# Kernel optimization log

Measured on AMD Instinct MI355X. Metric: run time of the kernel, lower is better.

The kernel has to match this reference:

```python
import jax, jax.numpy as jnp
import numpy as np

N = 50000
E = 800000
D = 128


def setup_inputs() -> dict:
    key = jax.random.key(0)
    ks = jax.random.split(key, 8)
    X = jax.random.normal(ks[0], (N, D), dtype=jnp.float32)
    edge_index = jax.random.randint(ks[1], (2, E), 0, N, dtype=jnp.int64)
    edge_weight = jax.random.uniform(ks[2], (E,), dtype=jnp.float32)
    # GCN weight (glorot-ish) and single-layer LSTM params (PyTorch layout).
    gcn_weight = jax.random.normal(ks[3], (D, D), dtype=jnp.float32) / np.sqrt(D)
    w_ih = jax.random.normal(ks[4], (4 * D, D), dtype=jnp.float32) / np.sqrt(D)
    w_hh = jax.random.normal(ks[5], (4 * D, D), dtype=jnp.float32) / np.sqrt(D)
    b_ih = jax.random.normal(ks[6], (4 * D,), dtype=jnp.float32) / np.sqrt(D)
    b_hh = jax.random.normal(ks[7], (4 * D,), dtype=jnp.float32) / np.sqrt(D)
    return {"X": X, "edge_index": edge_index, "edge_weight": edge_weight,
            "gcn_weight": gcn_weight, "w_ih": w_ih, "w_hh": w_hh,
            "b_ih": b_ih, "b_hh": b_hh}


def _lstm_evolve_weight(W, w_ih, w_hh, b_ih, b_hh):
    # One LSTM step on the weight matrix: seq_len=1, batch=D, input=D, h0=c0=0.
    # h0 contribution is zero but kept so w_hh participates in the graph.
    gates = W @ w_ih.T + jnp.zeros_like(W) @ w_hh.T + b_ih + b_hh  # [D, 4D]
    i, f, g, o = jnp.split(gates, 4, axis=-1)  # PyTorch gate order i,f,g,o
    c = jax.nn.sigmoid(i) * jnp.tanh(g)        # f * c0 = 0
    h = jax.nn.sigmoid(o) * jnp.tanh(c)
    return h  # new [D, D] weight


def reference(X, edge_index, edge_weight, gcn_weight, w_ih, w_hh, b_ih, b_hh):
    W = _lstm_evolve_weight(gcn_weight, w_ih, w_hh, b_ih, b_hh)
    n = X.shape[0]
    # GCNConv: add self-loops (weight 1), symmetric normalization.
    loop = jnp.arange(n, dtype=edge_index.dtype)
    row = jnp.concatenate([edge_index[0], loop])   # sources
    col = jnp.concatenate([edge_index[1], loop])   # targets (aggregation)
    ew = jnp.concatenate([edge_weight, jnp.ones((n,), dtype=edge_weight.dtype)])
    deg = jax.ops.segment_sum(ew, col, num_segments=n)
    dinv = jnp.where(deg > 0, jax.lax.rsqrt(jnp.maximum(deg, 1e-30)), 0.0)
    norm = dinv[row] * ew * dinv[col]              # [E+N]
    xw = X @ W                                     # [N, D] dense transform first
    out = jax.ops.segment_sum(norm[:, None] * xw[row], col, num_segments=n)
    return out
```

## Files before the change

kernel.cpp:

```cpp
#include <hip/hip_runtime.h>
#include <math.h>

#define N_NODES 50000
#define N_EDGES 800000
#define DIM 128
#define PART_SZ 6250
#define SUBCAP 32

typedef __attribute__((ext_vector_type(8))) short bf16x8;
typedef __attribute__((ext_vector_type(4))) float f32x4;
typedef __attribute__((ext_vector_type(4))) int i32x4;

__device__ inline unsigned short f2bf(float f) {
  unsigned int u = __builtin_bit_cast(unsigned int, f);
  u = (u + 0x7FFFu + ((u >> 16) & 1u)) >> 16;
  return (unsigned short)u;
}
__device__ inline float bflo(unsigned int v) {
  return __builtin_bit_cast(float, v << 16);
}
__device__ inline float bfhi(unsigned int v) {
  return __builtin_bit_cast(float, v & 0xffff0000u);
}

__global__ __launch_bounds__(256) void lstm_evolve(
    const float* __restrict__ gcn, const float* __restrict__ w_ih,
    const float* __restrict__ b_ih, const float* __restrict__ b_hh,
    unsigned short* __restrict__ Wt) {
  int idx = blockIdx.x * 256 + threadIdx.x;
  int r = idx >> 7;
  int c = idx & 127;
  const float4* g_row = (const float4*)(gcn + r * DIM);
  const float4* wi = (const float4*)(w_ih + (long)c * DIM);
  const float4* wg = (const float4*)(w_ih + (long)(c + 256) * DIM);
  const float4* wo = (const float4*)(w_ih + (long)(c + 384) * DIM);
  float ai = 0.f, ag = 0.f, ao = 0.f;
#pragma unroll 8
  for (int k = 0; k < DIM / 4; ++k) {
    float4 gv = g_row[k];
    float4 iv = wi[k], gg = wg[k], ov = wo[k];
    ai += gv.x * iv.x + gv.y * iv.y + gv.z * iv.z + gv.w * iv.w;
    ag += gv.x * gg.x + gv.y * gg.y + gv.z * gg.z + gv.w * gg.w;
    ao += gv.x * ov.x + gv.y * ov.y + gv.z * ov.z + gv.w * ov.w;
  }
  ai += b_ih[c] + b_hh[c];
  ag += b_ih[c + 256] + b_hh[c + 256];
  ao += b_ih[c + 384] + b_hh[c + 384];
  float si = 1.f / (1.f + expf(-ai));
  float so = 1.f / (1.f + expf(-ao));
  float cc = si * tanhf(ag);
  float h = so * tanhf(cc);
  Wt[c * DIM + r] = f2bf(h);
}

__global__ __launch_bounds__(256) void init_cursor(int* __restrict__ cursor) {
  int i = blockIdx.x * 256 + threadIdx.x;
  if (i < N_NODES * 2) cursor[i] = 0;
}

__device__ inline void put_edge(int c, long e, int src, float w,
                                int* __restrict__ cursor,
                                unsigned int* __restrict__ bkt) {
  int sub = (int)e & 1;
  int pos = atomicAdd(&cursor[c * 2 + sub], 1);
  if (pos < SUBCAP) {
    unsigned int pk = ((unsigned int)src << 16) | (unsigned int)f2bf(w);
    bkt[(long)c * 64 + sub * SUBCAP + pos] = pk;
  }
}

__global__ __launch_bounds__(256) void fill_buckets(
    const int* __restrict__ rows, const int* __restrict__ cols,
    const float* __restrict__ ew, int* __restrict__ cursor,
    unsigned int* __restrict__ bkt) {
  int part = blockIdx.x & 7;
  int lo = part * PART_SZ;
  int hi = lo + PART_SZ;
  long e0 = ((long)(blockIdx.x >> 3)) * 1024 + threadIdx.x * 4;
  if (e0 >= N_EDGES) return;
  i32x4 c = __builtin_nontemporal_load((const i32x4*)(cols + e0));
  if (c.x >= lo && c.x < hi) {
    int s = __builtin_nontemporal_load(rows + e0 + 0);
    float w = __builtin_nontemporal_load(ew + e0 + 0);
    put_edge(c.x, e0 + 0, s, w, cursor, bkt);
  }
  if (c.y >= lo && c.y < hi) {
    int s = __builtin_nontemporal_load(rows + e0 + 1);
    float w = __builtin_nontemporal_load(ew + e0 + 1);
    put_edge(c.y, e0 + 1, s, w, cursor, bkt);
  }
  if (c.z >= lo && c.z < hi) {
    int s = __builtin_nontemporal_load(rows + e0 + 2);
    float w = __builtin_nontemporal_load(ew + e0 + 2);
    put_edge(c.z, e0 + 2, s, w, cursor, bkt);
  }
  if (c.w >= lo && c.w < hi) {
    int s = __builtin_nontemporal_load(rows + e0 + 3);
    float w = __builtin_nontemporal_load(ew + e0 + 3);
    put_edge(c.w, e0 + 3, s, w, cursor, bkt);
  }
}

__global__ __launch_bounds__(256) void deg_dinv(
    const int2* __restrict__ cursor, const unsigned int* __restrict__ bkt,
    float* __restrict__ dinv) {
  int wave = threadIdx.x >> 6;
  int lane = threadIdx.x & 63;
  int node = blockIdx.x * 4 + wave;
  if (node >= N_NODES) return;
  int2 cc = cursor[node];
  int c0 = cc.x < SUBCAP ? cc.x : SUBCAP;
  int c1 = cc.y < SUBCAP ? cc.y : SUBCAP;
  int j = lane & 31;
  int cs = (lane >> 5) ? c1 : c0;
  float w = 0.f;
  if (j < cs) w = bflo(bkt[(long)node * 64 + lane]);
#pragma unroll
  for (int off = 32; off > 0; off >>= 1) w += __shfl_down(w, off, 64);
  if (lane == 0) dinv[node] = rsqrtf(1.0f + w);
}

__global__ __launch_bounds__(256) void gemm_mfma(
    const float* __restrict__ X, const unsigned short* __restrict__ Wt,
    unsigned short* __restrict__ xwb) {
  int wave = threadIdx.x >> 6;
  int lane = threadIdx.x & 63;
  long r0 = (long)blockIdx.x * 64 + wave * 16;
  int m = lane & 15;
  int kg = lane >> 4;
  long rA = r0 + m;
  if (rA >= N_NODES) rA = N_NODES - 1;
  const float* xrow = X + rA * DIM;
  bf16x8 a[4];
#pragma unroll
  for (int kt = 0; kt < 4; ++kt) {
    const float4* p = (const float4*)(xrow + kt * 32 + kg * 8);
    float4 lo = p[0], hi = p[1];
    bf16x8 f;
    f[0] = (short)f2bf(lo.x); f[1] = (short)f2bf(lo.y);
    f[2] = (short)f2bf(lo.z); f[3] = (short)f2bf(lo.w);
    f[4] = (short)f2bf(hi.x); f[5] = (short)f2bf(hi.y);
    f[6] = (short)f2bf(hi.z); f[7] = (short)f2bf(hi.w);
    a[kt] = f;
  }
#pragma unroll
  for (int nt = 0; nt < 8; ++nt) {
    f32x4 acc = {0.f, 0.f, 0.f, 0.f};
#pragma unroll
    for (int kt = 0; kt < 4; ++kt) {
      bf16x8 b = *(const bf16x8*)(Wt + (nt * 16 + m) * DIM + kt * 32 + kg * 8);
      acc = __builtin_amdgcn_mfma_f32_16x16x32_bf16(a[kt], b, acc, 0, 0, 0);
    }
#pragma unroll
    for (int reg = 0; reg < 4; ++reg) {
      long rr = r0 + kg * 4 + reg;
      if (rr < N_NODES) xwb[rr * DIM + nt * 16 + m] = f2bf(acc[reg]);
    }
  }
}

__global__ __launch_bounds__(256) void gather_nodes(
    const int2* __restrict__ cursor, const unsigned int* __restrict__ bkt,
    const unsigned short* __restrict__ xwb, const float* __restrict__ dinv,
    float* __restrict__ out) {
  int wave = threadIdx.x >> 6;
  int lane = threadIdx.x & 63;
  int node = blockIdx.x * 4 + wave;
  if (node >= N_NODES) return;
  int2 cc = cursor[node];
  int c0 = cc.x < SUBCAP ? cc.x : SUBCAP;
  int c1 = cc.y < SUBCAP ? cc.y : SUBCAP;
  int j = lane & 31;
  int cs = (lane >> 5) ? c1 : c0;

  int src_l = 0;
  float pre_l = 0.f;
  if (j < cs) {
    unsigned int pk = bkt[(long)node * 64 + lane];
    int s = pk >> 16;
    src_l = s;
    pre_l = dinv[s] * bflo(pk);
  }

  float ax = 0.f, ay = 0.f;
  int cmax = c0 > c1 ? c0 : c1;
  for (int i = 0; i < cmax; i += 2) {
    int sA = __shfl(src_l, i, 64);
    int sB = __shfl(src_l, i + 1, 64);
    int sC = __shfl(src_l, 32 + i, 64);
    int sD = __shfl(src_l, 33 + i, 64);
    float wA = __shfl(pre_l, i, 64);
    float wB = __shfl(pre_l, i + 1, 64);
    float wC = __shfl(pre_l, 32 + i, 64);
    float wD = __shfl(pre_l, 33 + i, 64);
    unsigned int vA = *(const unsigned int*)(xwb + ((long)sA << 7) + 2 * lane);
    unsigned int vB = *(const unsigned int*)(xwb + ((long)sB << 7) + 2 * lane);
    unsigned int vC = *(const unsigned int*)(xwb + ((long)sC << 7) + 2 * lane);
    unsigned int vD = *(const unsigned int*)(xwb + ((long)sD << 7) + 2 * lane);
    ax += wA * bflo(vA) + wB * bflo(vB) + wC * bflo(vC) + wD * bflo(vD);
    ay += wA * bfhi(vA) + wB * bfhi(vB) + wC * bfhi(vC) + wD * bfhi(vD);
  }
  float dv = dinv[node];
  unsigned int vs = *(const unsigned int*)(xwb + ((long)node << 7) + 2 * lane);
  float2 o;
  o.x = dv * (ax + dv * bflo(vs));
  o.y = dv * (ay + dv * bfhi(vs));
  ((float2*)out)[((long)node << 6) + lane] = o;
}

extern "C" void kernel_launch(void* const* d_in, const int* in_sizes, int n_in,
                              void* d_out, int out_size, void* d_ws,
                              size_t ws_size, hipStream_t stream) {
  const float* X = (const float*)d_in[0];
  const int* ei = (const int*)d_in[1];
  const float* ew = (const float*)d_in[2];
  const float* gcn = (const float*)d_in[3];
  const float* w_ih = (const float*)d_in[4];
  const float* b_ih = (const float*)d_in[6];
  const float* b_hh = (const float*)d_in[7];
  float* out = (float*)d_out;

  const int* e_row = ei;
  const int* e_col = ei + N_EDGES;

  char* ws = (char*)d_ws;
  unsigned short* Wt = (unsigned short*)(ws + 0);
  float* dinv = (float*)(ws + 65536);
  int* cursor = (int*)(ws + 270336);
  unsigned int* bkt = (unsigned int*)(ws + 679936);
  unsigned short* xwb = (unsigned short*)(ws + 13479936);

  lstm_evolve<<<64, 256, 0, stream>>>(gcn, w_ih, b_ih, b_hh, Wt);
  init_cursor<<<(N_NODES * 2 + 255) / 256, 256, 0, stream>>>(cursor);
  fill_buckets<<<8 * ((N_EDGES + 1023) / 1024), 256, 0, stream>>>(
      e_row, e_col, ew, cursor, bkt);
  deg_dinv<<<(N_NODES + 3) / 4, 256, 0, stream>>>((const int2*)cursor, bkt,
                                                  dinv);
  gemm_mfma<<<(N_NODES + 63) / 64, 256, 0, stream>>>(X, Wt, xwb);
  gather_nodes<<<(N_NODES + 3) / 4, 256, 0, stream>>>((const int2*)cursor, bkt,
                                                      xwb, dinv, out);
}
```

Baseline: 134.0 us.

## Fuse bucket fill with GEMM, fold cursor init into LSTM, unroll gather

Merges cursor zeroing into the LSTM weight-evolve kernel, and puts edge bucketing and the MFMA GEMM into one launch that splits blocks by index, cutting two kernel launches. Each fill block now handles four 1024-edge chunks and uses ordinary loads where it used nontemporal ones. The gather loop is unrolled to issue eight row loads per iteration for more memory-level parallelism. The cost is heterogeneous blocks in one grid and higher register pressure in the gather.

```diff
diff --git a/kernel.cpp b/kernel.cpp
--- a/kernel.cpp
+++ b/kernel.cpp
@@ -6,6 +6,8 @@
 #define DIM 128
 #define PART_SZ 6250
 #define SUBCAP 32
+#define FILLB 1568
+#define GEMMB 782
 
 typedef __attribute__((ext_vector_type(8))) short bf16x8;
 typedef __attribute__((ext_vector_type(4))) float f32x4;
@@ -26,8 +28,9 @@
 __global__ __launch_bounds__(256) void lstm_evolve(
     const float* __restrict__ gcn, const float* __restrict__ w_ih,
     const float* __restrict__ b_ih, const float* __restrict__ b_hh,
-    unsigned short* __restrict__ Wt) {
+    unsigned short* __restrict__ Wt, int* __restrict__ cursor) {
   int idx = blockIdx.x * 256 + threadIdx.x;
+  for (int i = idx; i < N_NODES * 2; i += 64 * 256) cursor[i] = 0;
   int r = idx >> 7;
   int c = idx & 127;
   const float4* g_row = (const float4*)(gcn + r * DIM);
@@ -53,11 +56,6 @@
   Wt[c * DIM + r] = f2bf(h);
 }
 
-__global__ __launch_bounds__(256) void init_cursor(int* __restrict__ cursor) {
-  int i = blockIdx.x * 256 + threadIdx.x;
-  if (i < N_NODES * 2) cursor[i] = 0;
-}
-
 __device__ inline void put_edge(int c, long e, int src, float w,
                                 int* __restrict__ cursor,
                                 unsigned int* __restrict__ bkt) {
@@ -69,35 +67,67 @@
   }
 }
 
-__global__ __launch_bounds__(256) void fill_buckets(
+__global__ __launch_bounds__(256) void fill_gemm(
     const int* __restrict__ rows, const int* __restrict__ cols,
     const float* __restrict__ ew, int* __restrict__ cursor,
-    unsigned int* __restrict__ bkt) {
-  int part = blockIdx.x & 7;
-  int lo = part * PART_SZ;
-  int hi = lo + PART_SZ;
-  long e0 = ((long)(blockIdx.x >> 3)) * 1024 + threadIdx.x * 4;
-  if (e0 >= N_EDGES) return;
-  i32x4 c = __builtin_nontemporal_load((const i32x4*)(cols + e0));
-  if (c.x >= lo && c.x < hi) {
-    int s = __builtin_nontemporal_load(rows + e0 + 0);
-    float w = __builtin_nontemporal_load(ew + e0 + 0);
-    put_edge(c.x, e0 + 0, s, w, cursor, bkt);
-  }
-  if (c.y >= lo && c.y < hi) {
-    int s = __builtin_nontemporal_load(rows + e0 + 1);
-    float w = __builtin_nontemporal_load(ew + e0 + 1);
-    put_edge(c.y, e0 + 1, s, w, cursor, bkt);
-  }
-  if (c.z >= lo && c.z < hi) {
-    int s = __builtin_nontemporal_load(rows + e0 + 2);
-    float w = __builtin_nontemporal_load(ew + e0 + 2);
-    put_edge(c.z, e0 + 2, s, w, cursor, bkt);
-  }
-  if (c.w >= lo && c.w < hi) {
-    int s = __builtin_nontemporal_load(rows + e0 + 3);
-    float w = __builtin_nontemporal_load(ew + e0 + 3);
-    put_edge(c.w, e0 + 3, s, w, cursor, bkt);
+    unsigned int* __restrict__ bkt, const float* __restrict__ X,
+    const unsigned short* __restrict__ Wt, unsigned short* __restrict__ xwb) {
+  int bid = blockIdx.x;
+  if (bid < FILLB) {
+    int part = bid & 7;
+    int lo = part * PART_SZ;
+    int hi = lo + PART_SZ;
+    long base = (long)(bid >> 3) * 4096;
+#pragma unroll
+    for (int j = 0; j < 4; ++j) {
+      long e0 = base + j * 1024 + threadIdx.x * 4;
+      if (e0 >= N_EDGES) continue;
+      i32x4 c = *(const i32x4*)(cols + e0);
+      if (c.x >= lo && c.x < hi)
+        put_edge(c.x, e0 + 0, rows[e0 + 0], ew[e0 + 0], cursor, bkt);
+      if (c.y >= lo && c.y < hi)
+        put_edge(c.y, e0 + 1, rows[e0 + 1], ew[e0 + 1], cursor, bkt);
+      if (c.z >= lo && c.z < hi)
+        put_edge(c.z, e0 + 2, rows[e0 + 2], ew[e0 + 2], cursor, bkt);
+      if (c.w >= lo && c.w < hi)
+        put_edge(c.w, e0 + 3, rows[e0 + 3], ew[e0 + 3], cursor, bkt);
+    }
+  } else {
+    int wave = threadIdx.x >> 6;
+    int lane = threadIdx.x & 63;
+    long r0 = (long)(bid - FILLB) * 64 + wave * 16;
+    int m = lane & 15;
+    int kg = lane >> 4;
+    long rA = r0 + m;
+    if (rA >= N_NODES) rA = N_NODES - 1;
+    const float* xrow = X + rA * DIM;
+    bf16x8 a[4];
+#pragma unroll
+    for (int kt = 0; kt < 4; ++kt) {
+      const float4* p = (const float4*)(xrow + kt * 32 + kg * 8);
+      float4 lo4 = p[0], hi4 = p[1];
+      bf16x8 f;
+      f[0] = (short)f2bf(lo4.x); f[1] = (short)f2bf(lo4.y);
+      f[2] = (short)f2bf(lo4.z); f[3] = (short)f2bf(lo4.w);
+      f[4] = (short)f2bf(hi4.x); f[5] = (short)f2bf(hi4.y);
+      f[6] = (short)f2bf(hi4.z); f[7] = (short)f2bf(hi4.w);
+      a[kt] = f;
+    }
+#pragma unroll
+    for (int nt = 0; nt < 8; ++nt) {
+      f32x4 acc = {0.f, 0.f, 0.f, 0.f};
+#pragma unroll
+      for (int kt = 0; kt < 4; ++kt) {
+        bf16x8 b =
+            *(const bf16x8*)(Wt + (nt * 16 + m) * DIM + kt * 32 + kg * 8);
+        acc = __builtin_amdgcn_mfma_f32_16x16x32_bf16(a[kt], b, acc, 0, 0, 0);
+      }
+#pragma unroll
+      for (int reg = 0; reg < 4; ++reg) {
+        long rr = r0 + kg * 4 + reg;
+        if (rr < N_NODES) xwb[rr * DIM + nt * 16 + m] = f2bf(acc[reg]);
+      }
+    }
   }
 }
 
@@ -120,45 +150,6 @@
   if (lane == 0) dinv[node] = rsqrtf(1.0f + w);
 }
 
-__global__ __launch_bounds__(256) void gemm_mfma(
-    const float* __restrict__ X, const unsigned short* __restrict__ Wt,
-    unsigned short* __restrict__ xwb) {
-  int wave = threadIdx.x >> 6;
-  int lane = threadIdx.x & 63;
-  long r0 = (long)blockIdx.x * 64 + wave * 16;
-  int m = lane & 15;
-  int kg = lane >> 4;
-  long rA = r0 + m;
-  if (rA >= N_NODES) rA = N_NODES - 1;
-  const float* xrow = X + rA * DIM;
-  bf16x8 a[4];
-#pragma unroll
-  for (int kt = 0; kt < 4; ++kt) {
-    const float4* p = (const float4*)(xrow + kt * 32 + kg * 8);
-    float4 lo = p[0], hi = p[1];
-    bf16x8 f;
-    f[0] = (short)f2bf(lo.x); f[1] = (short)f2bf(lo.y);
-    f[2] = (short)f2bf(lo.z); f[3] = (short)f2bf(lo.w);
-    f[4] = (short)f2bf(hi.x); f[5] = (short)f2bf(hi.y);
-    f[6] = (short)f2bf(hi.z); f[7] = (short)f2bf(hi.w);
-    a[kt] = f;
-  }
-#pragma unroll
-  for (int nt = 0; nt < 8; ++nt) {
-    f32x4 acc = {0.f, 0.f, 0.f, 0.f};
-#pragma unroll
-    for (int kt = 0; kt < 4; ++kt) {
-      bf16x8 b = *(const bf16x8*)(Wt + (nt * 16 + m) * DIM + kt * 32 + kg * 8);
-      acc = __builtin_amdgcn_mfma_f32_16x16x32_bf16(a[kt], b, acc, 0, 0, 0);
-    }
-#pragma unroll
-    for (int reg = 0; reg < 4; ++reg) {
-      long rr = r0 + kg * 4 + reg;
-      if (rr < N_NODES) xwb[rr * DIM + nt * 16 + m] = f2bf(acc[reg]);
-    }
-  }
-}
-
 __global__ __launch_bounds__(256) void gather_nodes(
     const int2* __restrict__ cursor, const unsigned int* __restrict__ bkt,
     const unsigned short* __restrict__ xwb, const float* __restrict__ dinv,
@@ -184,21 +175,35 @@
 
   float ax = 0.f, ay = 0.f;
   int cmax = c0 > c1 ? c0 : c1;
-  for (int i = 0; i < cmax; i += 2) {
-    int sA = __shfl(src_l, i, 64);
-    int sB = __shfl(src_l, i + 1, 64);
-    int sC = __shfl(src_l, 32 + i, 64);
-    int sD = __shfl(src_l, 33 + i, 64);
-    float wA = __shfl(pre_l, i, 64);
-    float wB = __shfl(pre_l, i + 1, 64);
-    float wC = __shfl(pre_l, 32 + i, 64);
-    float wD = __shfl(pre_l, 33 + i, 64);
-    unsigned int vA = *(const unsigned int*)(xwb + ((long)sA << 7) + 2 * lane);
-    unsigned int vB = *(const unsigned int*)(xwb + ((long)sB << 7) + 2 * lane);
-    unsigned int vC = *(const unsigned int*)(xwb + ((long)sC << 7) + 2 * lane);
-    unsigned int vD = *(const unsigned int*)(xwb + ((long)sD << 7) + 2 * lane);
-    ax += wA * bflo(vA) + wB * bflo(vB) + wC * bflo(vC) + wD * bflo(vD);
-    ay += wA * bfhi(vA) + wB * bfhi(vB) + wC * bfhi(vC) + wD * bfhi(vD);
+  for (int i = 0; i < cmax; i += 4) {
+    int s0 = __shfl(src_l, i, 64);
+    int s1 = __shfl(src_l, i + 1, 64);
+    int s2 = __shfl(src_l, i + 2, 64);
+    int s3 = __shfl(src_l, i + 3, 64);
+    int s4 = __shfl(src_l, 32 + i, 64);
+    int s5 = __shfl(src_l, 33 + i, 64);
+    int s6 = __shfl(src_l, 34 + i, 64);
+    int s7 = __shfl(src_l, 35 + i, 64);
+    float w0 = __shfl(pre_l, i, 64);
+    float w1 = __shfl(pre_l, i + 1, 64);
+    float w2 = __shfl(pre_l, i + 2, 64);
+    float w3 = __shfl(pre_l, i + 3, 64);
+    float w4 = __shfl(pre_l, 32 + i, 64);
+    float w5 = __shfl(pre_l, 33 + i, 64);
+    float w6 = __shfl(pre_l, 34 + i, 64);
+    float w7 = __shfl(pre_l, 35 + i, 64);
+    unsigned int v0 = *(const unsigned int*)(xwb + ((long)s0 << 7) + 2 * lane);
+    unsigned int v1 = *(const unsigned int*)(xwb + ((long)s1 << 7) + 2 * lane);
+    unsigned int v2 = *(const unsigned int*)(xwb + ((long)s2 << 7) + 2 * lane);
+    unsigned int v3 = *(const unsigned int*)(xwb + ((long)s3 << 7) + 2 * lane);
+    unsigned int v4 = *(const unsigned int*)(xwb + ((long)s4 << 7) + 2 * lane);
+    unsigned int v5 = *(const unsigned int*)(xwb + ((long)s5 << 7) + 2 * lane);
+    unsigned int v6 = *(const unsigned int*)(xwb + ((long)s6 << 7) + 2 * lane);
+    unsigned int v7 = *(const unsigned int*)(xwb + ((long)s7 << 7) + 2 * lane);
+    ax += w0 * bflo(v0) + w1 * bflo(v1) + w2 * bflo(v2) + w3 * bflo(v3) +
+          w4 * bflo(v4) + w5 * bflo(v5) + w6 * bflo(v6) + w7 * bflo(v7);
+    ay += w0 * bfhi(v0) + w1 * bfhi(v1) + w2 * bfhi(v2) + w3 * bfhi(v3) +
+          w4 * bfhi(v4) + w5 * bfhi(v5) + w6 * bfhi(v6) + w7 * bfhi(v7);
   }
   float dv = dinv[node];
   unsigned int vs = *(const unsigned int*)(xwb + ((long)node << 7) + 2 * lane);
@@ -230,13 +235,11 @@
   unsigned int* bkt = (unsigned int*)(ws + 679936);
   unsigned short* xwb = (unsigned short*)(ws + 13479936);
 
-  lstm_evolve<<<64, 256, 0, stream>>>(gcn, w_ih, b_ih, b_hh, Wt);
-  init_cursor<<<(N_NODES * 2 + 255) / 256, 256, 0, stream>>>(cursor);
-  fill_buckets<<<8 * ((N_EDGES + 1023) / 1024), 256, 0, stream>>>(
-      e_row, e_col, ew, cursor, bkt);
+  lstm_evolve<<<64, 256, 0, stream>>>(gcn, w_ih, b_ih, b_hh, Wt, cursor);
+  fill_gemm<<<FILLB + GEMMB, 256, 0, stream>>>(e_row, e_col, ew, cursor, bkt,
+                                               X, Wt, xwb);
   deg_dinv<<<(N_NODES + 3) / 4, 256, 0, stream>>>((const int2*)cursor, bkt,
                                                   dinv);
-  gemm_mfma<<<(N_NODES + 63) / 64, 256, 0, stream>>>(X, Wt, xwb);
   gather_nodes<<<(N_NODES + 3) / 4, 256, 0, stream>>>((const int2*)cursor, bkt,
                                                       xwb, dinv, out);
 }
```

New measurement: 112.5 us. 1.19x faster.
